# Optimization experiments

Hardware: AMD Instinct MI355X
Metric: run time of the kernel (lower is better)

Reference implementation:

```python
import jax, jax.numpy as jnp
import numpy as np

N_NODES = 100000
N_EDGES = 800000
IN_DIM = 128
HID = 128
N_CLASSES = 4


def setup_inputs() -> dict:
    key = jax.random.key(0)
    ks = jax.random.split(key, 8)
    x = jax.random.normal(ks[0], (N_NODES, IN_DIM), dtype=jnp.float32)
    edge_index = jax.random.randint(ks[1], (2, N_EDGES), 0, N_NODES, dtype=jnp.int32)
    s0 = 1.0 / np.sqrt(IN_DIM)
    s1 = 1.0 / np.sqrt(HID)
    W0 = jax.random.uniform(ks[2], (HID, IN_DIM), minval=-s0, maxval=s0, dtype=jnp.float32)
    b0 = jax.random.uniform(ks[3], (HID,), minval=-s0, maxval=s0, dtype=jnp.float32)
    W1 = jax.random.uniform(ks[4], (HID, HID), minval=-s1, maxval=s1, dtype=jnp.float32)
    b1 = jax.random.uniform(ks[5], (HID,), minval=-s1, maxval=s1, dtype=jnp.float32)
    Wc = jax.random.uniform(ks[6], (N_CLASSES, HID), minval=-s1, maxval=s1, dtype=jnp.float32)
    bc = jax.random.uniform(ks[7], (N_CLASSES,), minval=-s1, maxval=s1, dtype=jnp.float32)
    return {"x": x, "edge_index": edge_index, "W0": W0, "b0": b0,
            "W1": W1, "b1": b1, "Wc": Wc, "bc": bc}


def reference(x, edge_index, W0, b0, W1, b1, Wc, bc):
    row, col = edge_index[0], edge_index[1]
    n = x.shape[0]
    # layer 0: Linear + ReLU (dropout is identity in eval)
    h = jax.nn.relu(x @ W0.T + b0)                                  # [N, HID]
    # scatter-add neighbor aggregation with degree normalization
    agg = jax.ops.segment_sum(h[col], row, num_segments=n)          # [N, HID]
    deg = jax.ops.segment_sum(jnp.ones_like(row, dtype=h.dtype), row, num_segments=n)
    agg = agg / jnp.clip(deg, 1.0)[:, None]
    h = h + agg                                                     # residual add
    # final conv + ReLU + classifier
    h = jax.nn.relu(h @ W1.T + b1)
    logits = h @ Wc.T + bc                                          # [N, N_CLASSES]
    return logits
```

## Files before the change

kernel.cpp:

```cpp
#include <hip/hip_runtime.h>

#define IN_DIM 128
#define HID    128
#define NCLS   4

typedef __attribute__((ext_vector_type(8))) short bf16x8;
typedef __attribute__((ext_vector_type(4))) float f32x4;

__device__ inline ushort f2bf(float x) {
    uint u = __builtin_bit_cast(uint, x);
    u += 0x7FFFu + ((u >> 16) & 1u);
    return (ushort)(u >> 16);
}
__device__ inline float bf2f(ushort h) {
    uint u = ((uint)h) << 16;
    return __builtin_bit_cast(float, u);
}

__device__ inline void split8(const float4& x0, const float4& x1, bf16x8& h, bf16x8& l) {
    float v[8] = {x0.x, x0.y, x0.z, x0.w, x1.x, x1.y, x1.z, x1.w};
    #pragma unroll
    for (int j = 0; j < 8; ++j) {
        ushort hh = f2bf(v[j]);
        ushort ll = f2bf(v[j] - bf2f(hh));
        h[j] = (short)hh;
        l[j] = (short)ll;
    }
}

__global__ __launch_bounds__(256) void cast_w(const float* __restrict__ W0,
                                              const float* __restrict__ W1,
                                              ushort* __restrict__ w0h, ushort* __restrict__ w0l,
                                              ushort* __restrict__ w1h, ushort* __restrict__ w1l)
{
    int i = blockIdx.x * 256 + threadIdx.x;
    float v = (i < 16384) ? W0[i] : W1[i - 16384];
    ushort h = f2bf(v);
    ushort l = f2bf(v - bf2f(h));
    if (i < 16384) { w0h[i] = h; w0l[i] = l; }
    else           { w1h[i - 16384] = h; w1l[i - 16384] = l; }
}

__global__ __launch_bounds__(256) void gnn_lin0_mfma(const float* __restrict__ X,
                                                     const ushort* __restrict__ Whi,
                                                     const ushort* __restrict__ Wlo,
                                                     const float* __restrict__ Bv,
                                                     ushort* __restrict__ Hhi,
                                                     ushort* __restrict__ Hlo, int M)
{
    const int tid = threadIdx.x;
    const int wid = tid >> 6, lane = tid & 63;
    const int wr = wid >> 1, wc = wid & 1;
    const int rowbase = blockIdx.x * 64 + wr * 32;
    const int colbase = wc * 64;
    const int lr = lane & 15, lk = lane >> 4;

    f32x4 acc[4][2];
    #pragma unroll
    for (int nt = 0; nt < 4; ++nt)
        #pragma unroll
        for (int rt = 0; rt < 2; ++rt) acc[nt][rt] = (f32x4){0.f, 0.f, 0.f, 0.f};

    const float4* X4 = (const float4*)X;

    #pragma unroll
    for (int kt = 0; kt < 4; ++kt) {
        const int ko = kt * 32 + lk * 8;
        bf16x8 xh[2], xl[2];
        #pragma unroll
        for (int rt = 0; rt < 2; ++rt) {
            int row = rowbase + rt * 16 + lr;
            float4 x0 = make_float4(0.f, 0.f, 0.f, 0.f);
            float4 x1 = x0;
            if (row < M) {
                size_t base = (size_t)row * 32 + (ko >> 2);
                x0 = X4[base];
                x1 = X4[base + 1];
            }
            split8(x0, x1, xh[rt], xl[rt]);
        }
        #pragma unroll
        for (int nt = 0; nt < 4; ++nt) {
            size_t bo = (size_t)(colbase + nt * 16 + lr) * 128 + ko;
            bf16x8 wh = *(const bf16x8*)(Whi + bo);
            bf16x8 wl = *(const bf16x8*)(Wlo + bo);
            #pragma unroll
            for (int rt = 0; rt < 2; ++rt) {
                acc[nt][rt] = __builtin_amdgcn_mfma_f32_16x16x32_bf16(wh, xh[rt], acc[nt][rt], 0, 0, 0);
                acc[nt][rt] = __builtin_amdgcn_mfma_f32_16x16x32_bf16(wh, xl[rt], acc[nt][rt], 0, 0, 0);
                acc[nt][rt] = __builtin_amdgcn_mfma_f32_16x16x32_bf16(wl, xh[rt], acc[nt][rt], 0, 0, 0);
            }
        }
    }

    #pragma unroll
    for (int nt = 0; nt < 4; ++nt) {
        const int col0 = colbase + nt * 16 + lk * 4;
        const float4 bv4 = *(const float4*)(Bv + col0);
        const float bvv[4] = {bv4.x, bv4.y, bv4.z, bv4.w};
        #pragma unroll
        for (int rt = 0; rt < 2; ++rt) {
            int row = rowbase + rt * 16 + lr;
            ushort4 h4, l4;
            float o0 = fmaxf(acc[nt][rt][0] + bvv[0], 0.f);
            float o1 = fmaxf(acc[nt][rt][1] + bvv[1], 0.f);
            float o2 = fmaxf(acc[nt][rt][2] + bvv[2], 0.f);
            float o3 = fmaxf(acc[nt][rt][3] + bvv[3], 0.f);
            h4.x = f2bf(o0); l4.x = f2bf(o0 - bf2f(h4.x));
            h4.y = f2bf(o1); l4.y = f2bf(o1 - bf2f(h4.y));
            h4.z = f2bf(o2); l4.z = f2bf(o2 - bf2f(h4.z));
            h4.w = f2bf(o3); l4.w = f2bf(o3 - bf2f(h4.w));
            size_t oo = (size_t)row * 128 + col0;
            *(ushort4*)(Hhi + oo) = h4;
            *(ushort4*)(Hlo + oo) = l4;
        }
    }
}

__global__ __launch_bounds__(256) void gnn_lin1_mfma(const ushort* __restrict__ Ahi,
                                                     const ushort* __restrict__ Alo,
                                                     const ushort* __restrict__ Whi,
                                                     const ushort* __restrict__ Wlo,
                                                     const float* __restrict__ Bv,
                                                     const float* __restrict__ Wc,
                                                     const float* __restrict__ bc,
                                                     float* __restrict__ Out, int M)
{
    __shared__ float red[2][64][4];

    const int tid = threadIdx.x;
    const int wid = tid >> 6, lane = tid & 63;
    const int wr = wid >> 1, wc = wid & 1;
    const int rowbase = blockIdx.x * 64 + wr * 32;
    const int colbase = wc * 64;
    const int lr = lane & 15, lk = lane >> 4;

    f32x4 acc[4][2];
    #pragma unroll
    for (int nt = 0; nt < 4; ++nt)
        #pragma unroll
        for (int rt = 0; rt < 2; ++rt) acc[nt][rt] = (f32x4){0.f, 0.f, 0.f, 0.f};

    #pragma unroll
    for (int kt = 0; kt < 4; ++kt) {
        const int ko = kt * 32 + lk * 8;
        bf16x8 xh[2], xl[2];
        #pragma unroll
        for (int rt = 0; rt < 2; ++rt) {
            size_t ao = (size_t)(rowbase + rt * 16 + lr) * 128 + ko;
            xh[rt] = *(const bf16x8*)(Ahi + ao);
            xl[rt] = *(const bf16x8*)(Alo + ao);
        }
        #pragma unroll
        for (int nt = 0; nt < 4; ++nt) {
            size_t bo = (size_t)(colbase + nt * 16 + lr) * 128 + ko;
            bf16x8 wh = *(const bf16x8*)(Whi + bo);
            bf16x8 wl = *(const bf16x8*)(Wlo + bo);
            #pragma unroll
            for (int rt = 0; rt < 2; ++rt) {
                acc[nt][rt] = __builtin_amdgcn_mfma_f32_16x16x32_bf16(wh, xh[rt], acc[nt][rt], 0, 0, 0);
                acc[nt][rt] = __builtin_amdgcn_mfma_f32_16x16x32_bf16(wh, xl[rt], acc[nt][rt], 0, 0, 0);
                acc[nt][rt] = __builtin_amdgcn_mfma_f32_16x16x32_bf16(wl, xh[rt], acc[nt][rt], 0, 0, 0);
            }
        }
    }

    float p[2][4] = {{0.f, 0.f, 0.f, 0.f}, {0.f, 0.f, 0.f, 0.f}};
    #pragma unroll
    for (int nt = 0; nt < 4; ++nt) {
        const int col0 = colbase + nt * 16 + lk * 4;
        const float4 bv4 = *(const float4*)(Bv + col0);
        const float bvv[4] = {bv4.x, bv4.y, bv4.z, bv4.w};
        float4 wcr[4];
        #pragma unroll
        for (int c = 0; c < 4; ++c) wcr[c] = *(const float4*)(Wc + c * HID + col0);
        #pragma unroll
        for (int rt = 0; rt < 2; ++rt) {
            float h2v[4];
            #pragma unroll
            for (int r = 0; r < 4; ++r) h2v[r] = fmaxf(acc[nt][rt][r] + bvv[r], 0.f);
            #pragma unroll
            for (int c = 0; c < 4; ++c) {
                const float* w = (const float*)&wcr[c];
                p[rt][c] = fmaf(h2v[0], w[0], p[rt][c]);
                p[rt][c] = fmaf(h2v[1], w[1], p[rt][c]);
                p[rt][c] = fmaf(h2v[2], w[2], p[rt][c]);
                p[rt][c] = fmaf(h2v[3], w[3], p[rt][c]);
            }
        }
    }
    #pragma unroll
    for (int off = 16; off < 64; off <<= 1)
        #pragma unroll
        for (int rt = 0; rt < 2; ++rt)
            #pragma unroll
            for (int c = 0; c < 4; ++c)
                p[rt][c] += __shfl_xor(p[rt][c], off);

    if (lk == 0) {
        #pragma unroll
        for (int rt = 0; rt < 2; ++rt) {
            f32x4 v = {p[rt][0], p[rt][1], p[rt][2], p[rt][3]};
            *(f32x4*)&red[wc][wr * 32 + rt * 16 + lr][0] = v;
        }
    }
    __syncthreads();

    const int row_local = tid >> 2, cls = tid & 3;
    int row = blockIdx.x * 64 + row_local;
    if (row < M) {
        float s = bc[cls] + red[0][row_local][cls] + red[1][row_local][cls];
        Out[(size_t)row * 4 + cls] = s;
    }
}

__global__ __launch_bounds__(256) void count_deg(const int* __restrict__ rows,
                                                 int* __restrict__ deg, int E)
{
    int e = blockIdx.x * 256 + threadIdx.x;
    if (e < E) atomicAdd(&deg[rows[e]], 1);
}

__global__ __launch_bounds__(256) void scan_blocks(const int* __restrict__ deg,
                                                   int* __restrict__ off,
                                                   int* __restrict__ bsum, int M)
{
    __shared__ int sh[256];
    int i = blockIdx.x * 256 + threadIdx.x;
    int v = (i < M) ? deg[i] : 0;
    sh[threadIdx.x] = v;
    __syncthreads();
    #pragma unroll
    for (int d = 1; d < 256; d <<= 1) {
        int t = (threadIdx.x >= d) ? sh[threadIdx.x - d] : 0;
        __syncthreads();
        sh[threadIdx.x] += t;
        __syncthreads();
    }
    if (i < M) off[i] = sh[threadIdx.x] - v;
    if (threadIdx.x == 255) bsum[blockIdx.x] = sh[255];
}

__global__ __launch_bounds__(512) void scan_bsum(int* __restrict__ bsum, int NB)
{
    __shared__ int sh[512];
    int v = (threadIdx.x < NB) ? bsum[threadIdx.x] : 0;
    sh[threadIdx.x] = v;
    __syncthreads();
    #pragma unroll
    for (int d = 1; d < 512; d <<= 1) {
        int t = (threadIdx.x >= d) ? sh[threadIdx.x - d] : 0;
        __syncthreads();
        sh[threadIdx.x] += t;
        __syncthreads();
    }
    if (threadIdx.x < NB) bsum[threadIdx.x] = sh[threadIdx.x] - v;
}

__global__ __launch_bounds__(256) void add_off(int* __restrict__ off,
                                               const int* __restrict__ bsum,
                                               int* __restrict__ pos, int M)
{
    int i = blockIdx.x * 256 + threadIdx.x;
    if (i < M) {
        int o = off[i] + bsum[i >> 8];
        off[i] = o;
        pos[i] = o;
    }
}

__global__ __launch_bounds__(256) void fill_csr(const int* __restrict__ rows,
                                                const int* __restrict__ cols,
                                                int* __restrict__ pos,
                                                int* __restrict__ col_sorted, int E)
{
    int e = blockIdx.x * 256 + threadIdx.x;
    if (e < E) {
        int p = atomicAdd(&pos[rows[e]], 1);
        col_sorted[p] = cols[e];
    }
}

__global__ __launch_bounds__(256) void gnn_aggregate(const ushort* __restrict__ Hhi,
                                                     const ushort* __restrict__ Hlo,
                                                     const int* __restrict__ off,
                                                     const int* __restrict__ deg,
                                                     const int* __restrict__ col_sorted,
                                                     ushort* __restrict__ InHi,
                                                     ushort* __restrict__ InLo,
                                                     int M, int Mpad)
{
    int gid  = blockIdx.x * 8 + (threadIdx.x >> 5);
    int lane = threadIdx.x & 31;
    if (gid >= Mpad) return;
    size_t oidx = (size_t)gid * 32 + lane;
    if (gid >= M) {
        ((ushort4*)InHi)[oidx] = make_ushort4(0, 0, 0, 0);
        ((ushort4*)InLo)[oidx] = make_ushort4(0, 0, 0, 0);
        return;
    }

    const ushort4* G = (const ushort4*)Hhi;
    int start = off[gid];
    int d     = deg[gid];
    int end   = start + d;

    float a0 = 0.f, a1 = 0.f, a2 = 0.f, a3 = 0.f;
    float b0 = 0.f, b1 = 0.f, b2 = 0.f, b3 = 0.f;
    int e = start;
    for (; e + 2 <= end; e += 2) {
        int c0 = col_sorted[e];
        int c1 = col_sorted[e + 1];
        ushort4 g0 = G[(size_t)c0 * 32 + lane];
        ushort4 g1 = G[(size_t)c1 * 32 + lane];
        a0 += bf2f(g0.x); a1 += bf2f(g0.y); a2 += bf2f(g0.z); a3 += bf2f(g0.w);
        b0 += bf2f(g1.x); b1 += bf2f(g1.y); b2 += bf2f(g1.z); b3 += bf2f(g1.w);
    }
    if (e < end) {
        int c0 = col_sorted[e];
        ushort4 g0 = G[(size_t)c0 * 32 + lane];
        a0 += bf2f(g0.x); a1 += bf2f(g0.y); a2 += bf2f(g0.z); a3 += bf2f(g0.w);
    }
    a0 += b0; a1 += b1; a2 += b2; a3 += b3;

    float inv = 1.0f / fmaxf((float)d, 1.0f);
    ushort4 rh = ((const ushort4*)Hhi)[oidx];
    ushort4 rl = ((const ushort4*)Hlo)[oidx];
    float o0 = bf2f(rh.x) + bf2f(rl.x) + a0 * inv;
    float o1 = bf2f(rh.y) + bf2f(rl.y) + a1 * inv;
    float o2 = bf2f(rh.z) + bf2f(rl.z) + a2 * inv;
    float o3 = bf2f(rh.w) + bf2f(rl.w) + a3 * inv;

    ushort4 h4, l4;
    h4.x = f2bf(o0); l4.x = f2bf(o0 - bf2f(h4.x));
    h4.y = f2bf(o1); l4.y = f2bf(o1 - bf2f(h4.y));
    h4.z = f2bf(o2); l4.z = f2bf(o2 - bf2f(h4.z));
    h4.w = f2bf(o3); l4.w = f2bf(o3 - bf2f(h4.w));
    ((ushort4*)InHi)[oidx] = h4;
    ((ushort4*)InLo)[oidx] = l4;
}

extern "C" void kernel_launch(void* const* d_in, const int* in_sizes, int n_in,
                              void* d_out, int out_size, void* d_ws, size_t ws_size,
                              hipStream_t stream)
{
    const float* x  = (const float*)d_in[0];
    const int*   ei = (const int*)  d_in[1];
    const float* W0 = (const float*)d_in[2];
    const float* b0 = (const float*)d_in[3];
    const float* W1 = (const float*)d_in[4];
    const float* b1 = (const float*)d_in[5];
    const float* Wc = (const float*)d_in[6];
    const float* bc = (const float*)d_in[7];
    float* out = (float*)d_out;

    const int M    = in_sizes[0] / IN_DIM;
    const int E    = in_sizes[1] / 2;
    const int Mpad = (M + 63) & ~63;
    const int NB   = (M + 255) / 256;

    ushort* Hhi  = (ushort*)d_ws;
    ushort* Hlo  = Hhi  + (size_t)Mpad * 128;
    ushort* InHi = Hlo  + (size_t)Mpad * 128;
    ushort* InLo = InHi + (size_t)Mpad * 128;
    ushort* W0h  = InLo + (size_t)Mpad * 128;
    ushort* W0l  = W0h + 16384;
    ushort* W1h  = W0l + 16384;
    ushort* W1l  = W1h + 16384;
    int* deg_i   = (int*)(W1l + 16384);
    int* off     = deg_i + M;
    int* pos     = off + M;
    int* bsum    = pos + M;
    int* col_sorted = bsum + 512;

    const int* rows = ei;
    const int* cols = ei + E;

    hipMemsetAsync(deg_i, 0, (size_t)M * sizeof(int), stream);

    const int gridMM = Mpad / 64;
    const int gridE  = (E + 255) / 256;
    const int gridN  = (M + 255) / 256;

    cast_w<<<128, 256, 0, stream>>>(W0, W1, W0h, W0l, W1h, W1l);
    gnn_lin0_mfma<<<gridMM, 256, 0, stream>>>(x, W0h, W0l, b0, Hhi, Hlo, M);

    count_deg<<<gridE, 256, 0, stream>>>(rows, deg_i, E);
    scan_blocks<<<gridN, 256, 0, stream>>>(deg_i, off, bsum, M);
    scan_bsum<<<1, 512, 0, stream>>>(bsum, NB);
    add_off<<<gridN, 256, 0, stream>>>(off, bsum, pos, M);
    fill_csr<<<gridE, 256, 0, stream>>>(rows, cols, pos, col_sorted, E);

    gnn_aggregate<<<(Mpad + 7) / 8, 256, 0, stream>>>(Hhi, Hlo, off, deg_i, col_sorted,
                                                      InHi, InLo, M, Mpad);
    gnn_lin1_mfma<<<gridMM, 256, 0, stream>>>(InHi, InLo, W1h, W1l, b1, Wc, bc, out, M);
}
```

Before: 319.8 us.

## Stage activation tiles in swizzled LDS and unroll neighbor gather by four

Both linear kernels now stage the 64-row activation tile into XOR-swizzled shared memory before the MFMA loop, so each element is read and split once per block instead of once per wave column. lin0 does the split to bf16 hi/lo once per element, and lin1 uses direct global-to-LDS loads. The aggregation kernel's edge loop is unrolled from two to four independent accumulators, giving more gathers in flight. This adds a block-wide barrier and about 32KB of LDS per block, which may reduce occupancy.

```diff
diff --git a/kernel.cpp b/kernel.cpp
--- a/kernel.cpp
+++ b/kernel.cpp
@@ -17,15 +17,9 @@
     return __builtin_bit_cast(float, u);
 }
 
-__device__ inline void split8(const float4& x0, const float4& x1, bf16x8& h, bf16x8& l) {
-    float v[8] = {x0.x, x0.y, x0.z, x0.w, x1.x, x1.y, x1.z, x1.w};
-    #pragma unroll
-    for (int j = 0; j < 8; ++j) {
-        ushort hh = f2bf(v[j]);
-        ushort ll = f2bf(v[j] - bf2f(hh));
-        h[j] = (short)hh;
-        l[j] = (short)ll;
-    }
+__device__ inline void gload_lds16(const void* g, void* l) {
+    __builtin_amdgcn_global_load_lds((const __attribute__((address_space(1))) void*)g,
+                                     (__attribute__((address_space(3))) void*)l, 16, 0, 0);
 }
 
 __global__ __launch_bounds__(256) void cast_w(const float* __restrict__ W0,
@@ -41,6 +35,7 @@
     else           { w1h[i - 16384] = h; w1l[i - 16384] = l; }
 }
 
+
 __global__ __launch_bounds__(256) void gnn_lin0_mfma(const float* __restrict__ X,
                                                      const ushort* __restrict__ Whi,
                                                      const ushort* __restrict__ Wlo,
@@ -48,10 +43,45 @@
                                                      ushort* __restrict__ Hhi,
                                                      ushort* __restrict__ Hlo, int M)
 {
+    __shared__ uint4 lds4[2048];
+    char* lds = (char*)lds4;
+
     const int tid = threadIdx.x;
+    const int bm  = blockIdx.x * 64;
+
+    {
+        const int row  = tid >> 2;
+        const int seg  = tid & 3;
+        const int grow = min(bm + row, M - 1);
+        const float4* src = (const float4*)((const char*)X + (size_t)grow * 512 + seg * 128);
+        float4 v[8];
+        #pragma unroll
+        for (int j = 0; j < 8; ++j) v[j] = src[j];
+
+        #pragma unroll
+        for (int j = 0; j < 4; ++j) {
+            uint hw[4], lw[4];
+            #pragma unroll
+            for (int q = 0; q < 2; ++q) {
+                const float4 f = v[j * 2 + q];
+                ushort h0 = f2bf(f.x), h1 = f2bf(f.y), h2 = f2bf(f.z), h3 = f2bf(f.w);
+                ushort l0 = f2bf(f.x - bf2f(h0)), l1 = f2bf(f.y - bf2f(h1));
+                ushort l2 = f2bf(f.z - bf2f(h2)), l3 = f2bf(f.w - bf2f(h3));
+                hw[q * 2]     = (uint)h0 | ((uint)h1 << 16);
+                hw[q * 2 + 1] = (uint)h2 | ((uint)h3 << 16);
+                lw[q * 2]     = (uint)l0 | ((uint)l1 << 16);
+                lw[q * 2 + 1] = (uint)l2 | ((uint)l3 << 16);
+            }
+            int unit = (seg * 4 + j) ^ (row & 7);
+            int off  = row * 256 + unit * 16;
+            *(uint4*)(lds + off)         = make_uint4(hw[0], hw[1], hw[2], hw[3]);
+            *(uint4*)(lds + 16384 + off) = make_uint4(lw[0], lw[1], lw[2], lw[3]);
+        }
+    }
+    __syncthreads();
+
     const int wid = tid >> 6, lane = tid & 63;
     const int wr = wid >> 1, wc = wid & 1;
-    const int rowbase = blockIdx.x * 64 + wr * 32;
     const int colbase = wc * 64;
     const int lr = lane & 15, lk = lane >> 4;
 
@@ -60,8 +90,6 @@
     for (int nt = 0; nt < 4; ++nt)
         #pragma unroll
         for (int rt = 0; rt < 2; ++rt) acc[nt][rt] = (f32x4){0.f, 0.f, 0.f, 0.f};
-
-    const float4* X4 = (const float4*)X;
 
     #pragma unroll
     for (int kt = 0; kt < 4; ++kt) {
@@ -69,15 +97,11 @@
         bf16x8 xh[2], xl[2];
         #pragma unroll
         for (int rt = 0; rt < 2; ++rt) {
-            int row = rowbase + rt * 16 + lr;
-            float4 x0 = make_float4(0.f, 0.f, 0.f, 0.f);
-            float4 x1 = x0;
-            if (row < M) {
-                size_t base = (size_t)row * 32 + (ko >> 2);
-                x0 = X4[base];
-                x1 = X4[base + 1];
-            }
-            split8(x0, x1, xh[rt], xl[rt]);
+            int lrow = wr * 32 + rt * 16 + lr;
+            int unit = (kt * 4 + lk) ^ (lrow & 7);
+            int off  = lrow * 256 + unit * 16;
+            xh[rt] = *(const bf16x8*)(lds + off);
+            xl[rt] = *(const bf16x8*)(lds + 16384 + off);
         }
         #pragma unroll
         for (int nt = 0; nt < 4; ++nt) {
@@ -100,12 +124,12 @@
         const float bvv[4] = {bv4.x, bv4.y, bv4.z, bv4.w};
         #pragma unroll
         for (int rt = 0; rt < 2; ++rt) {
-            int row = rowbase + rt * 16 + lr;
-            ushort4 h4, l4;
+            int row = bm + wr * 32 + rt * 16 + lr;
             float o0 = fmaxf(acc[nt][rt][0] + bvv[0], 0.f);
             float o1 = fmaxf(acc[nt][rt][1] + bvv[1], 0.f);
             float o2 = fmaxf(acc[nt][rt][2] + bvv[2], 0.f);
             float o3 = fmaxf(acc[nt][rt][3] + bvv[3], 0.f);
+            ushort4 h4, l4;
             h4.x = f2bf(o0); l4.x = f2bf(o0 - bf2f(h4.x));
             h4.y = f2bf(o1); l4.y = f2bf(o1 - bf2f(h4.y));
             h4.z = f2bf(o2); l4.z = f2bf(o2 - bf2f(h4.z));
@@ -126,12 +150,28 @@
                                                      const float* __restrict__ bc,
                                                      float* __restrict__ Out, int M)
 {
+    __shared__ uint4 lds4[2048];
     __shared__ float red[2][64][4];
+    char* lds = (char*)lds4;
 
     const int tid = threadIdx.x;
     const int wid = tid >> 6, lane = tid & 63;
+    const int bm  = blockIdx.x * 64;
+
+    #pragma unroll
+    for (int i = 0; i < 8; ++i) {
+        int o = wid * 8192 + i * 1024 + lane * 16;
+        const ushort* plane = (o < 16384) ? Ahi : Alo;
+        int po   = o & 16383;
+        int row  = po >> 8;
+        int unit = (po >> 4) & 15;
+        const char* src = (const char*)plane + (size_t)(bm + row) * 256
+                        + ((unit ^ (row & 7)) << 4);
+        gload_lds16(src, lds + wid * 8192 + i * 1024);
+    }
+    __syncthreads();
+
     const int wr = wid >> 1, wc = wid & 1;
-    const int rowbase = blockIdx.x * 64 + wr * 32;
     const int colbase = wc * 64;
     const int lr = lane & 15, lk = lane >> 4;
 
@@ -147,9 +187,11 @@
         bf16x8 xh[2], xl[2];
         #pragma unroll
         for (int rt = 0; rt < 2; ++rt) {
-            size_t ao = (size_t)(rowbase + rt * 16 + lr) * 128 + ko;
-            xh[rt] = *(const bf16x8*)(Ahi + ao);
-            xl[rt] = *(const bf16x8*)(Alo + ao);
+            int lrow = wr * 32 + rt * 16 + lr;
+            int unit = (kt * 4 + lk) ^ (lrow & 7);
+            int off  = lrow * 256 + unit * 16;
+            xh[rt] = *(const bf16x8*)(lds + off);
+            xl[rt] = *(const bf16x8*)(lds + 16384 + off);
         }
         #pragma unroll
         for (int nt = 0; nt < 4; ++nt) {
@@ -305,23 +347,32 @@
     int d     = deg[gid];
     int end   = start + d;
 
-    float a0 = 0.f, a1 = 0.f, a2 = 0.f, a3 = 0.f;
-    float b0 = 0.f, b1 = 0.f, b2 = 0.f, b3 = 0.f;
+    float s0[4] = {0.f, 0.f, 0.f, 0.f};
+    float s1[4] = {0.f, 0.f, 0.f, 0.f};
+    float s2[4] = {0.f, 0.f, 0.f, 0.f};
+    float s3[4] = {0.f, 0.f, 0.f, 0.f};
     int e = start;
-    for (; e + 2 <= end; e += 2) {
-        int c0 = col_sorted[e];
-        int c1 = col_sorted[e + 1];
+    for (; e + 4 <= end; e += 4) {
+        int c0 = col_sorted[e], c1 = col_sorted[e + 1];
+        int c2 = col_sorted[e + 2], c3 = col_sorted[e + 3];
         ushort4 g0 = G[(size_t)c0 * 32 + lane];
         ushort4 g1 = G[(size_t)c1 * 32 + lane];
-        a0 += bf2f(g0.x); a1 += bf2f(g0.y); a2 += bf2f(g0.z); a3 += bf2f(g0.w);
-        b0 += bf2f(g1.x); b1 += bf2f(g1.y); b2 += bf2f(g1.z); b3 += bf2f(g1.w);
-    }
-    if (e < end) {
+        ushort4 g2 = G[(size_t)c2 * 32 + lane];
+        ushort4 g3 = G[(size_t)c3 * 32 + lane];
+        s0[0] += bf2f(g0.x); s0[1] += bf2f(g0.y); s0[2] += bf2f(g0.z); s0[3] += bf2f(g0.w);
+        s1[0] += bf2f(g1.x); s1[1] += bf2f(g1.y); s1[2] += bf2f(g1.z); s1[3] += bf2f(g1.w);
+        s2[0] += bf2f(g2.x); s2[1] += bf2f(g2.y); s2[2] += bf2f(g2.z); s2[3] += bf2f(g2.w);
+        s3[0] += bf2f(g3.x); s3[1] += bf2f(g3.y); s3[2] += bf2f(g3.z); s3[3] += bf2f(g3.w);
+    }
+    for (; e < end; ++e) {
         int c0 = col_sorted[e];
         ushort4 g0 = G[(size_t)c0 * 32 + lane];
-        a0 += bf2f(g0.x); a1 += bf2f(g0.y); a2 += bf2f(g0.z); a3 += bf2f(g0.w);
-    }
-    a0 += b0; a1 += b1; a2 += b2; a3 += b3;
+        s0[0] += bf2f(g0.x); s0[1] += bf2f(g0.y); s0[2] += bf2f(g0.z); s0[3] += bf2f(g0.w);
+    }
+    float a0 = (s0[0] + s1[0]) + (s2[0] + s3[0]);
+    float a1 = (s0[1] + s1[1]) + (s2[1] + s3[1]);
+    float a2 = (s0[2] + s1[2]) + (s2[2] + s3[2]);
+    float a3 = (s0[3] + s1[3]) + (s2[3] + s3[3]);
 
     float inv = 1.0f / fmaxf((float)d, 1.0f);
     ushort4 rh = ((const ushort4*)Hhi)[oidx];
```

New measurement: 309.3 us. 3.3% less time.
